# Kernel optimization log

Measured on AMD Instinct MI355X. Metric: run time of the kernel, lower is better.

Reference implementation:

```python
import jax, jax.numpy as jnp
import numpy as np
import math

D_MODEL = 1024
N_HEADS = 16
D_HEAD = D_MODEL // N_HEADS
D_FF = 4 * D_MODEL
EPS = 1e-5


def layer_norm(x, gamma, beta):
    mu = jnp.mean(x, axis=-1, keepdims=True)
    var = jnp.var(x, axis=-1, keepdims=True)
    return (x - mu) * jax.lax.rsqrt(var + EPS) * gamma + beta


def setup_inputs() -> dict:
    key = jax.random.key(0)
    ks = jax.random.split(key, 8)
    B, C, D = 32, 256, D_MODEL
    s = 0.02
    return {
        "X": jax.random.normal(ks[0], (B, C, D), dtype=jnp.float32),
        "W_qkv": jax.random.normal(ks[1], (D, 3 * D), dtype=jnp.float32) * s,
        "b_qkv": jnp.zeros((3 * D,), dtype=jnp.float32),
        "W_proj": jax.random.normal(ks[2], (D, D), dtype=jnp.float32) * s,
        "b_proj": jnp.zeros((D,), dtype=jnp.float32),
        "g1": jnp.ones((D,), dtype=jnp.float32),
        "beta1": jnp.zeros((D,), dtype=jnp.float32),
        "g2": jnp.ones((D,), dtype=jnp.float32),
        "beta2": jnp.zeros((D,), dtype=jnp.float32),
        "W_ff1": jax.random.normal(ks[3], (D, D_FF), dtype=jnp.float32) * s,
        "b_ff1": jnp.zeros((D_FF,), dtype=jnp.float32),
        "W_ff2": jax.random.normal(ks[4], (D_FF, D), dtype=jnp.float32) * s,
        "b_ff2": jnp.zeros((D,), dtype=jnp.float32),
    }


def reference(X, W_qkv, b_qkv, W_proj, b_proj, g1, beta1, g2, beta2,
              W_ff1, b_ff1, W_ff2, b_ff2):
    B, C, D = X.shape
    H, Dh = N_HEADS, D_HEAD
    scale = 1.0 / math.sqrt(Dh)

    Xn = layer_norm(X, g1, beta1)
    qkv = Xn @ W_qkv + b_qkv                       # [B, C, 3D]
    q, k, v = jnp.split(qkv, 3, axis=-1)
    # split heads -> [B, H, C, Dh]
    sh = lambda t: t.reshape(B, C, H, Dh).transpose(0, 2, 1, 3)
    q, k, v = sh(q), sh(k), sh(v)

    scores = jnp.einsum("bhcd,bhkd->bhck", q, k) * scale  # [B, H, C, C]
    attn = jax.nn.softmax(scores, axis=-1)
    ctx = jnp.einsum("bhck,bhkd->bhcd", attn, v)           # [B, H, C, Dh]
    ctx = ctx.transpose(0, 2, 1, 3).reshape(B, C, D)

    X1 = X + (ctx @ W_proj + b_proj)
    X2n = layer_norm(X1, g2, beta2)
    h = jax.nn.gelu(X2n @ W_ff1 + b_ff1, approximate=False)
    X_out = X1 + (h @ W_ff2 + b_ff2)
    A = attn.mean(axis=1)                                   # [B, C, C]
    return (X_out, A)
```

## Files before the change

kernel.cpp:

```cpp
#include <hip/hip_runtime.h>
#include <cstdint>
#include <cstddef>

typedef short bf16x8 __attribute__((ext_vector_type(8)));
typedef float f32x4 __attribute__((ext_vector_type(4)));
typedef unsigned short u16;
typedef u16 u16x8 __attribute__((ext_vector_type(8)));

#define GLD16(gptr, lptr)                                                            \
  __builtin_amdgcn_global_load_lds((const __attribute__((address_space(1))) void*)(gptr), \
                                   (__attribute__((address_space(3))) void*)(lptr), 16, 0, 0)

__device__ __forceinline__ u16 f2bf(float f) {
  union { float f; unsigned u; } v; v.f = f;
  unsigned r = v.u + 0x7FFF + ((v.u >> 16) & 1);
  return (u16)(r >> 16);
}
__device__ __forceinline__ float bf2f(u16 h) {
  union { unsigned u; float f; } v; v.u = ((unsigned)h) << 16;
  return v.f;
}

__device__ __forceinline__ bf16x8 lds_read_sw64(const u16* base, int row, int col) {
  int byt = row * 128 + col * 2;
  byt ^= (row & 7) << 4;
  return *(const bf16x8*)((const char*)base + byt);
}

__global__ __launch_bounds__(256) void transpose_cast(const float* __restrict__ in,
                                                      u16* __restrict__ out, int R, int C) {
  __shared__ float tile[32][33];
  const int tx = threadIdx.x, ty = threadIdx.y;
  const int c0 = blockIdx.x * 32, r0 = blockIdx.y * 32;
#pragma unroll
  for (int i = 0; i < 32; i += 8)
    tile[ty + i][tx] = in[(size_t)(r0 + ty + i) * C + c0 + tx];
  __syncthreads();
#pragma unroll
  for (int i = 0; i < 32; i += 8)
    out[(size_t)(c0 + ty + i) * R + r0 + tx] = f2bf(tile[tx][ty + i]);
}

__global__ __launch_bounds__(256) void layernorm_bf16(const float* __restrict__ X,
                                                      const float* __restrict__ g,
                                                      const float* __restrict__ be,
                                                      u16* __restrict__ out) {
  const int row = blockIdx.x, t = threadIdx.x;
  const int lane = t & 63, wave = t >> 6;
  const float* x = X + (size_t)row * 1024;
  __shared__ float part[4];
  float v[4]; float s = 0.f;
#pragma unroll
  for (int i = 0; i < 4; ++i) { v[i] = x[t + i * 256]; s += v[i]; }
#pragma unroll
  for (int o = 32; o >= 1; o >>= 1) s += __shfl_xor(s, o);
  if (lane == 0) part[wave] = s;
  __syncthreads();
  const float mu = (part[0] + part[1] + part[2] + part[3]) * (1.f / 1024.f);
  float d2 = 0.f;
#pragma unroll
  for (int i = 0; i < 4; ++i) { float d = v[i] - mu; d2 += d * d; }
#pragma unroll
  for (int o = 32; o >= 1; o >>= 1) d2 += __shfl_xor(d2, o);
  __syncthreads();
  if (lane == 0) part[wave] = d2;
  __syncthreads();
  const float var = (part[0] + part[1] + part[2] + part[3]) * (1.f / 1024.f);
  const float rstd = rsqrtf(var + 1e-5f);
#pragma unroll
  for (int i = 0; i < 4; ++i) {
    const int c = t + i * 256;
    out[(size_t)row * 1024 + c] = f2bf((v[i] - mu) * rstd * g[c] + be[c]);
  }
}

template <int EPI>
__global__ __launch_bounds__(256, 2) void gemm_sb(const u16* __restrict__ A,
                                                  const u16* __restrict__ Bt,
                                                  const float* __restrict__ bias,
                                                  const float* __restrict__ res,
                                                  float* __restrict__ outf,
                                                  u16* __restrict__ outb,
                                                  int M, int N, int K) {
  constexpr int ABYT = 128 * 128;
  __shared__ __attribute__((aligned(16))) char lds[2 * ABYT];

  const int t = threadIdx.x, lane = t & 63, wave = t >> 6;
  const int wm = wave >> 1, wn = wave & 1;
  const int l15 = lane & 15, l16 = lane >> 4;

  const int xcd = (int)blockIdx.x & 7, q = (int)blockIdx.x >> 3;
  const int j = q & 63, gq = q >> 6;
  const int g = gq * 8 + xcd;
  const int NGN = N >> 10;
  const int gm = g / NGN, gn = g % NGN;
  const int bm = (gm * 8 + (j >> 3)) * 128;
  const int bn = (gn * 8 + (j & 7)) * 128;

  const u16* aptr[4];
  const u16* bptr[4];
#pragma unroll
  for (int c = 0; c < 4; ++c) {
    int Lb = c * 4096 + t * 16;
    int x = (Lb ^ ((Lb >> 3) & 0x70)) >> 1;
    aptr[c] = A + (size_t)(bm + (x >> 6)) * K + (x & 63);
    bptr[c] = Bt + (size_t)(bn + (x >> 6)) * K + (x & 63);
  }

  auto stage = [&](int p) {
    const int ko = p * 64;
    char* ab = lds + t * 16;
    char* bb = lds + ABYT + t * 16;
#pragma unroll
    for (int c = 0; c < 4; ++c) GLD16(aptr[c] + ko, ab + c * 4096);
#pragma unroll
    for (int c = 0; c < 4; ++c) GLD16(bptr[c] + ko, bb + c * 4096);
  };

  const int co0 = l16 * 16, co1 = 64 + l16 * 16;
  f32x4 acc[4][4] = {};
  const int nkt = K >> 6;

#pragma unroll 1
  for (int kt = 0; kt < nkt; ++kt) {
    __syncthreads();
    stage(kt);
    __syncthreads();

    const char* ab = lds;
    const char* bb = lds + ABYT;
#pragma unroll
    for (int ks = 0; ks < 2; ++ks) {
      const int co = ks ? co1 : co0;
      bf16x8 a[4], b[4];
#pragma unroll
      for (int m = 0; m < 4; ++m) {
        const int r = wm * 64 + m * 16 + l15;
        a[m] = *(const bf16x8*)(ab + r * 128 + (co ^ ((r & 7) << 4)));
      }
#pragma unroll
      for (int n = 0; n < 4; ++n) {
        const int r = wn * 64 + n * 16 + l15;
        b[n] = *(const bf16x8*)(bb + r * 128 + (co ^ ((r & 7) << 4)));
      }
#pragma unroll
      for (int m = 0; m < 4; ++m)
#pragma unroll
        for (int n = 0; n < 4; ++n)
          acc[m][n] = __builtin_amdgcn_mfma_f32_16x16x32_bf16(a[m], b[n], acc[m][n], 0, 0, 0);
    }
  }

  const int r0 = l16 * 4;
#pragma unroll
  for (int m = 0; m < 4; ++m) {
#pragma unroll
    for (int n = 0; n < 4; ++n) {
      const int col = bn + wn * 64 + n * 16 + l15;
      const float bv = bias[col];
#pragma unroll
      for (int r = 0; r < 4; ++r) {
        const int row = bm + wm * 64 + m * 16 + r0 + r;
        const float v = acc[m][n][r] + bv;
        const size_t o = (size_t)row * N + col;
        if (EPI == 0) {
          outb[o] = f2bf(v);
        } else if (EPI == 1) {
          outf[o] = res[o] + v;
        } else {
          const float u = 0.7978845608f * (v + 0.044715f * v * v * v);
          const float e = __expf(2.f * u);
          const float th = 1.f - 2.f / (1.f + e);
          outb[o] = f2bf(0.5f * v * (1.f + th));
        }
      }
    }
  }
}

__global__ __launch_bounds__(256) void attn_scores(const u16* __restrict__ qkv,
                                                   u16* __restrict__ probs) {
  __shared__ u16 Ks[256 * 64];
  __shared__ u16 Qs[64 * 64];
  const int t = threadIdx.x, lane = t & 63, wave = t >> 6;
  const int qb = blockIdx.x * 64, h = blockIdx.y, b = blockIdx.z;
  const size_t row0 = (size_t)b * 256 * 3072;

#pragma unroll
  for (int is = 0; is < 8; ++is) {
    int L = (is * 2048 + t * 8) * 2;
    int x = (L ^ ((L >> 3) & 0x70)) >> 1;
    int kk = x >> 6, d = x & 63;
    const u16* gp = qkv + row0 + (size_t)kk * 3072 + 1024 + h * 64 + d;
    GLD16(gp, (char*)Ks + is * 4096 + wave * 1024);
  }
#pragma unroll
  for (int is = 0; is < 2; ++is) {
    int L = (is * 2048 + t * 8) * 2;
    int x = (L ^ ((L >> 3) & 0x70)) >> 1;
    int q = x >> 6, d = x & 63;
    const u16* gp = qkv + row0 + (size_t)(qb + q) * 3072 + h * 64 + d;
    GLD16(gp, (char*)Qs + is * 4096 + wave * 1024);
  }
  __syncthreads();

  f32x4 acc[16] = {};
  bf16x8 aq[2];
#pragma unroll
  for (int ks = 0; ks < 2; ++ks)
    aq[ks] = lds_read_sw64(Qs, wave * 16 + (lane & 15), ks * 32 + (lane >> 4) * 8);
#pragma unroll
  for (int nf = 0; nf < 16; ++nf) {
#pragma unroll
    for (int ks = 0; ks < 2; ++ks) {
      bf16x8 bk = lds_read_sw64(Ks, nf * 16 + (lane & 15), ks * 32 + (lane >> 4) * 8);
      acc[nf] = __builtin_amdgcn_mfma_f32_16x16x32_bf16(aq[ks], bk, acc[nf], 0, 0, 0);
    }
  }

  const int r0 = (lane >> 4) * 4, cc = lane & 15;
  const float sc = 0.125f;
#pragma unroll
  for (int r = 0; r < 4; ++r) {
    float mx = -1e30f;
#pragma unroll
    for (int nf = 0; nf < 16; ++nf) mx = fmaxf(mx, acc[nf][r]);
#pragma unroll
    for (int o = 8; o >= 1; o >>= 1) mx = fmaxf(mx, __shfl_xor(mx, o));
    float s = 0.f;
#pragma unroll
    for (int nf = 0; nf < 16; ++nf) {
      float e = __expf((acc[nf][r] - mx) * sc);
      acc[nf][r] = e; s += e;
    }
#pragma unroll
    for (int o = 8; o >= 1; o >>= 1) s += __shfl_xor(s, o);
    const float rinv = 1.f / s;
    const int qrow = qb + wave * 16 + r0 + r;
    u16* prow = probs + (size_t)((b * 16 + h) * 256 + qrow) * 256;
#pragma unroll
    for (int nf = 0; nf < 16; ++nf)
      prow[nf * 16 + cc] = f2bf(acc[nf][r] * rinv);
  }
}

__global__ __launch_bounds__(256) void amean(const u16* __restrict__ probs,
                                             float* __restrict__ A) {
  const int bq = blockIdx.x;
  const int b = bq >> 8, q = bq & 255;
  const int t = threadIdx.x;
  float s = 0.f;
#pragma unroll
  for (int h = 0; h < 16; ++h)
    s += bf2f(probs[(size_t)((b * 16 + h) * 256 + q) * 256 + t]);
  A[(size_t)bq * 256 + t] = s * (1.f / 16.f);
}

__global__ __launch_bounds__(256) void attn_pv(const u16* __restrict__ qkv,
                                               const u16* __restrict__ probs,
                                               u16* __restrict__ ctx) {
  __shared__ u16 Vs[64 * 256];
  const int t = threadIdx.x, lane = t & 63, wave = t >> 6;
  const int h = blockIdx.x, b = blockIdx.y;

#pragma unroll
  for (int p = 0; p < 8; ++p) {
    int idx = p * 2048 + t * 8;
    int kk = idx >> 6, d0 = idx & 63;
    u16x8 vv = *(const u16x8*)(qkv + (size_t)(b * 256 + kk) * 3072 + 2048 + h * 64 + d0);
#pragma unroll
    for (int j = 0; j < 8; ++j) {
      int d = d0 + j;
      int byt = (d * 512 + kk * 2) ^ ((d & 7) << 4);
      *(u16*)((char*)Vs + byt) = vv[j];
    }
  }
  __syncthreads();

  f32x4 acc[4][4] = {};
  const u16* Pb = probs + (size_t)((b * 16 + h) * 256) * 256;
  const int cc = lane & 15, kg = (lane >> 4) * 8;
#pragma unroll
  for (int kt = 0; kt < 8; ++kt) {
    bf16x8 a[4], v[4];
#pragma unroll
    for (int m = 0; m < 4; ++m)
      a[m] = *(const bf16x8*)(Pb + (size_t)(wave * 64 + m * 16 + cc) * 256 + kt * 32 + kg);
#pragma unroll
    for (int n = 0; n < 4; ++n) {
      int d = n * 16 + cc;
      int kk = kt * 32 + kg;
      int byt = (d * 512 + kk * 2) ^ ((d & 7) << 4);
      v[n] = *(const bf16x8*)((const char*)Vs + byt);
    }
#pragma unroll
    for (int m = 0; m < 4; ++m)
#pragma unroll
      for (int n = 0; n < 4; ++n)
        acc[m][n] = __builtin_amdgcn_mfma_f32_16x16x32_bf16(a[m], v[n], acc[m][n], 0, 0, 0);
  }

  const int r0 = (lane >> 4) * 4;
#pragma unroll
  for (int m = 0; m < 4; ++m) {
    const int q = wave * 64 + m * 16 + r0;
#pragma unroll
    for (int n = 0; n < 4; ++n) {
      const int col = h * 64 + n * 16 + cc;
#pragma unroll
      for (int r = 0; r < 4; ++r)
        ctx[(size_t)(b * 256 + q + r) * 1024 + col] = f2bf(acc[m][n][r]);
    }
  }
}

extern "C" void kernel_launch(void* const* d_in, const int* in_sizes, int n_in,
                              void* d_out, int out_size, void* d_ws, size_t ws_size,
                              hipStream_t stream) {
  const float* X      = (const float*)d_in[0];
  const float* W_qkv  = (const float*)d_in[1];
  const float* b_qkv  = (const float*)d_in[2];
  const float* W_proj = (const float*)d_in[3];
  const float* b_proj = (const float*)d_in[4];
  const float* g1     = (const float*)d_in[5];
  const float* beta1  = (const float*)d_in[6];
  const float* g2     = (const float*)d_in[7];
  const float* beta2  = (const float*)d_in[8];
  const float* W_ff1  = (const float*)d_in[9];
  const float* b_ff1  = (const float*)d_in[10];
  const float* W_ff2  = (const float*)d_in[11];
  const float* b_ff2  = (const float*)d_in[12];

  float* Xout = (float*)d_out;
  float* Aout = (float*)d_out + 8388608;

  char* ws = (char*)d_ws;
  const size_t MB = 1u << 20;
  u16* xn    = (u16*)(ws + 0);
  u16* wqkv  = (u16*)(ws + 16 * MB);
  u16* wproj = (u16*)(ws + 22 * MB);
  u16* wff1  = (u16*)(ws + 24 * MB);
  u16* wff2  = (u16*)(ws + 32 * MB);
  u16* qkv   = (u16*)(ws + 40 * MB);
  u16* probs = (u16*)(ws + 88 * MB);
  u16* hbuf  = probs;
  float* x1  = (float*)(ws + 152 * MB);
  u16* ctx   = xn;
  u16* x1n   = xn;

  const dim3 tb(32, 8);
  transpose_cast<<<dim3(96, 32),  tb, 0, stream>>>(W_qkv,  wqkv, 1024, 3072);
  transpose_cast<<<dim3(32, 32),  tb, 0, stream>>>(W_proj, wproj, 1024, 1024);
  transpose_cast<<<dim3(128, 32), tb, 0, stream>>>(W_ff1,  wff1, 1024, 4096);
  transpose_cast<<<dim3(32, 128), tb, 0, stream>>>(W_ff2,  wff2, 4096, 1024);

  layernorm_bf16<<<8192, 256, 0, stream>>>(X, g1, beta1, xn);

  gemm_sb<0><<<1536, 256, 0, stream>>>(xn, wqkv, b_qkv, nullptr, nullptr, qkv,
                                       8192, 3072, 1024);

  attn_scores<<<dim3(4, 16, 32), 256, 0, stream>>>(qkv, probs);
  amean<<<8192, 256, 0, stream>>>(probs, Aout);
  attn_pv<<<dim3(16, 32), 256, 0, stream>>>(qkv, probs, ctx);

  gemm_sb<1><<<512, 256, 0, stream>>>(ctx, wproj, b_proj, X, x1, nullptr,
                                      8192, 1024, 1024);

  layernorm_bf16<<<8192, 256, 0, stream>>>(x1, g2, beta2, x1n);

  gemm_sb<2><<<2048, 256, 0, stream>>>(x1n, wff1, b_ff1, nullptr, nullptr, hbuf,
                                       8192, 4096, 1024);

  gemm_sb<1><<<512, 256, 0, stream>>>(hbuf, wff2, b_ff2, x1, Xout, nullptr,
                                      8192, 1024, 4096);
}
```

Baseline: 350.4 us.

## Add 256x256 ping-pong GEMM kernel for QKV and FF1 projections

Adds a new 512-thread GEMM with 256x256 output tiles and double-buffered LDS filled by direct global-to-LDS loads. The global loads for the next K tile are split across barrier-separated phases so they overlap the MFMA work, with raised priority around MFMA bursts. The kernel also remaps block indices for L2 locality. It replaces the 128x128 kernel for the QKV and FF1 GEMMs to increase data reuse per tile and reduce LDS/global traffic per flop. The cost is higher register pressure and fewer blocks per CU, and its hand-tuned waitcnt values have to match the issued loads exactly.

```diff
diff --git a/kernel.cpp b/kernel.cpp
--- a/kernel.cpp
+++ b/kernel.cpp
@@ -19,6 +19,16 @@
 __device__ __forceinline__ float bf2f(u16 h) {
   union { unsigned u; float f; } v; v.u = ((unsigned)h) << 16;
   return v.f;
+}
+
+template <int N> __device__ __forceinline__ void vmwait() {
+  if constexpr (N == 0) asm volatile("s_waitcnt vmcnt(0)" ::: "memory");
+  else if constexpr (N == 2) asm volatile("s_waitcnt vmcnt(2)" ::: "memory");
+  else asm volatile("s_waitcnt vmcnt(8)" ::: "memory");
+}
+
+__device__ __forceinline__ f32x4 mfma16(bf16x8 a, bf16x8 b, f32x4 c) {
+  return __builtin_amdgcn_mfma_f32_16x16x32_bf16(a, b, c, 0, 0, 0);
 }
 
 __device__ __forceinline__ bf16x8 lds_read_sw64(const u16* base, int row, int col) {
@@ -71,6 +81,158 @@
   for (int i = 0; i < 4; ++i) {
     const int c = t + i * 256;
     out[(size_t)row * 1024 + c] = f2bf((v[i] - mu) * rstd * g[c] + be[c]);
+  }
+}
+
+template <int EPI>
+__global__ __launch_bounds__(512, 2) void gemm_4p(const u16* __restrict__ A,
+                                                  const u16* __restrict__ Bt,
+                                                  const float* __restrict__ bias,
+                                                  const float* __restrict__ res,
+                                                  float* __restrict__ outf,
+                                                  u16* __restrict__ outb,
+                                                  int M, int N, int K) {
+  constexpr int TSZ = 256 * 128;
+  __shared__ __attribute__((aligned(16))) char lds[4 * TSZ];
+
+  const int t = threadIdx.x, lane = t & 63, wave = t >> 6;
+  const int wm = wave >> 2, wn = wave & 3;
+  const int l15 = lane & 15, l16 = lane >> 4;
+
+  const int lb = ((int)blockIdx.x & 7) * ((int)gridDim.x >> 3) + ((int)blockIdx.x >> 3);
+  const int NBN = N >> 8;
+  const int bm = (lb / NBN) * 256, bn = (lb % NBN) * 256;
+
+  const u16* aptr[4];
+  const u16* bptr[4];
+#pragma unroll
+  for (int u = 0; u < 4; ++u) {
+    int Lb = u * 8192 + t * 16;
+    int x = (Lb ^ ((Lb >> 3) & 0x70)) >> 1;
+    aptr[u] = A + (size_t)(bm + (x >> 6)) * K + (x & 63);
+    bptr[u] = Bt + (size_t)(bn + (x >> 6)) * K + (x & 63);
+  }
+  auto stA = [&](int p, int u) { GLD16(aptr[u] + p * 64, lds + (p & 1) * TSZ + u * 8192 + t * 16); };
+  auto stB = [&](int p, int u) { GLD16(bptr[u] + p * 64, lds + 2 * TSZ + (p & 1) * TSZ + u * 8192 + t * 16); };
+
+  stA(0, 0); stA(0, 2); stB(0, 0); stB(0, 1); stB(0, 2); stB(0, 3); stA(0, 1); stA(0, 3);
+
+  f32x4 acc[8][4] = {};
+  const int nkt = K >> 6;
+
+#pragma unroll 1
+  for (int kt = 0; kt < nkt; ++kt) {
+    const char* ab = lds + (kt & 1) * TSZ;
+    const char* bb = lds + 2 * TSZ + (kt & 1) * TSZ;
+    const bool st = (kt + 1 < nkt);
+    bf16x8 aF[4][2], b0[2][2], b1[2][2];
+
+    vmwait<2>();
+    asm volatile("s_barrier" ::: "memory");
+    if (st) { stA(kt + 1, 0); stA(kt + 1, 2); stB(kt + 1, 0); stB(kt + 1, 1); }
+#pragma unroll
+    for (int fm = 0; fm < 4; ++fm) {
+      const int r = wm * 128 + fm * 16 + l15;
+      const int rb = r * 128, sw = (r & 7) << 4;
+      aF[fm][0] = *(const bf16x8*)(ab + rb + ((l16 * 16) ^ sw));
+      aF[fm][1] = *(const bf16x8*)(ab + rb + ((64 + l16 * 16) ^ sw));
+    }
+#pragma unroll
+    for (int fn = 0; fn < 2; ++fn) {
+      const int r = wn * 64 + fn * 16 + l15;
+      const int rb = r * 128, sw = (r & 7) << 4;
+      b0[fn][0] = *(const bf16x8*)(bb + rb + ((l16 * 16) ^ sw));
+      b0[fn][1] = *(const bf16x8*)(bb + rb + ((64 + l16 * 16) ^ sw));
+    }
+    asm volatile("s_waitcnt lgkmcnt(0)" ::: "memory");
+    __builtin_amdgcn_sched_barrier(0);
+    __builtin_amdgcn_s_setprio(1);
+#pragma unroll
+    for (int ks = 0; ks < 2; ++ks)
+#pragma unroll
+      for (int fm = 0; fm < 4; ++fm)
+#pragma unroll
+        for (int fn = 0; fn < 2; ++fn)
+          acc[fm][fn] = mfma16(aF[fm][ks], b0[fn][ks], acc[fm][fn]);
+    __builtin_amdgcn_s_setprio(0);
+
+    asm volatile("s_barrier" ::: "memory");
+    if (st) { stB(kt + 1, 2); stB(kt + 1, 3); stA(kt + 1, 1); stA(kt + 1, 3); }
+#pragma unroll
+    for (int fn = 0; fn < 2; ++fn) {
+      const int r = wn * 64 + (2 + fn) * 16 + l15;
+      const int rb = r * 128, sw = (r & 7) << 4;
+      b1[fn][0] = *(const bf16x8*)(bb + rb + ((l16 * 16) ^ sw));
+      b1[fn][1] = *(const bf16x8*)(bb + rb + ((64 + l16 * 16) ^ sw));
+    }
+    asm volatile("s_waitcnt lgkmcnt(0)" ::: "memory");
+    __builtin_amdgcn_sched_barrier(0);
+    __builtin_amdgcn_s_setprio(1);
+#pragma unroll
+    for (int ks = 0; ks < 2; ++ks)
+#pragma unroll
+      for (int fm = 0; fm < 4; ++fm)
+#pragma unroll
+        for (int fn = 0; fn < 2; ++fn)
+          acc[fm][2 + fn] = mfma16(aF[fm][ks], b1[fn][ks], acc[fm][2 + fn]);
+    __builtin_amdgcn_s_setprio(0);
+
+    if (st) vmwait<8>(); else vmwait<0>();
+    asm volatile("s_barrier" ::: "memory");
+#pragma unroll
+    for (int fm = 0; fm < 4; ++fm) {
+      const int r = wm * 128 + (4 + fm) * 16 + l15;
+      const int rb = r * 128, sw = (r & 7) << 4;
+      aF[fm][0] = *(const bf16x8*)(ab + rb + ((l16 * 16) ^ sw));
+      aF[fm][1] = *(const bf16x8*)(ab + rb + ((64 + l16 * 16) ^ sw));
+    }
+    asm volatile("s_waitcnt lgkmcnt(0)" ::: "memory");
+    __builtin_amdgcn_sched_barrier(0);
+    __builtin_amdgcn_s_setprio(1);
+#pragma unroll
+    for (int ks = 0; ks < 2; ++ks)
+#pragma unroll
+      for (int fm = 0; fm < 4; ++fm)
+#pragma unroll
+        for (int fn = 0; fn < 2; ++fn)
+          acc[4 + fm][2 + fn] = mfma16(aF[fm][ks], b1[fn][ks], acc[4 + fm][2 + fn]);
+    __builtin_amdgcn_s_setprio(0);
+
+    __builtin_amdgcn_s_setprio(1);
+#pragma unroll
+    for (int ks = 0; ks < 2; ++ks)
+#pragma unroll
+      for (int fm = 0; fm < 4; ++fm)
+#pragma unroll
+        for (int fn = 0; fn < 2; ++fn)
+          acc[4 + fm][fn] = mfma16(aF[fm][ks], b0[fn][ks], acc[4 + fm][fn]);
+    __builtin_amdgcn_s_setprio(0);
+  }
+
+  const int r0 = l16 * 4;
+#pragma unroll
+  for (int fm = 0; fm < 8; ++fm) {
+#pragma unroll
+    for (int fn = 0; fn < 4; ++fn) {
+      const int col = bn + wn * 64 + fn * 16 + l15;
+      const float bv = bias[col];
+#pragma unroll
+      for (int r = 0; r < 4; ++r) {
+        const int row = bm + wm * 128 + fm * 16 + r0 + r;
+        const float v = acc[fm][fn][r] + bv;
+        const size_t o = (size_t)row * N + col;
+        if (EPI == 0) {
+          outb[o] = f2bf(v);
+        } else if (EPI == 1) {
+          outf[o] = res[o] + v;
+        } else {
+          const float u = 0.7978845608f * (v + 0.044715f * v * v * v);
+          const float e = __expf(2.f * u);
+          const float th = 1.f - 2.f / (1.f + e);
+          outb[o] = f2bf(0.5f * v * (1.f + th));
+        }
+      }
+    }
   }
 }
 
@@ -147,7 +309,7 @@
       for (int m = 0; m < 4; ++m)
 #pragma unroll
         for (int n = 0; n < 4; ++n)
-          acc[m][n] = __builtin_amdgcn_mfma_f32_16x16x32_bf16(a[m], b[n], acc[m][n], 0, 0, 0);
+          acc[m][n] = mfma16(a[m], b[n], acc[m][n]);
     }
   }
 
@@ -214,7 +376,7 @@
 #pragma unroll
     for (int ks = 0; ks < 2; ++ks) {
       bf16x8 bk = lds_read_sw64(Ks, nf * 16 + (lane & 15), ks * 32 + (lane >> 4) * 8);
-      acc[nf] = __builtin_amdgcn_mfma_f32_16x16x32_bf16(aq[ks], bk, acc[nf], 0, 0, 0);
+      acc[nf] = mfma16(aq[ks], bk, acc[nf]);
     }
   }
 
@@ -297,7 +459,7 @@
     for (int m = 0; m < 4; ++m)
 #pragma unroll
       for (int n = 0; n < 4; ++n)
-        acc[m][n] = __builtin_amdgcn_mfma_f32_16x16x32_bf16(a[m], v[n], acc[m][n], 0, 0, 0);
+        acc[m][n] = mfma16(a[m], v[n], acc[m][n]);
   }
 
   const int r0 = (lane >> 4) * 4;
@@ -356,8 +518,8 @@
 
   layernorm_bf16<<<8192, 256, 0, stream>>>(X, g1, beta1, xn);
 
-  gemm_sb<0><<<1536, 256, 0, stream>>>(xn, wqkv, b_qkv, nullptr, nullptr, qkv,
-                                       8192, 3072, 1024);
+  gemm_4p<0><<<384, 512, 0, stream>>>(xn, wqkv, b_qkv, nullptr, nullptr, qkv,
+                                      8192, 3072, 1024);
 
   attn_scores<<<dim3(4, 16, 32), 256, 0, stream>>>(qkv, probs);
   amean<<<8192, 256, 0, stream>>>(probs, Aout);
@@ -368,8 +530,8 @@
 
   layernorm_bf16<<<8192, 256, 0, stream>>>(x1, g2, beta2, x1n);
 
-  gemm_sb<2><<<2048, 256, 0, stream>>>(x1n, wff1, b_ff1, nullptr, nullptr, hbuf,
-                                       8192, 4096, 1024);
+  gemm_4p<2><<<512, 512, 0, stream>>>(x1n, wff1, b_ff1, nullptr, nullptr, hbuf,
+                                      8192, 4096, 1024);
 
   gemm_sb<1><<<512, 256, 0, stream>>>(hbuf, wff2, b_ff2, x1, Xout, nullptr,
                                       8192, 1024, 4096);
```

Result: slower. 357.4 us (+2.0%).

## Fuse attention scores, softmax, head-mean and PV into one per-query-block kernel

Applied to the files above, without the earlier changes.

Replaces the separate score/softmax, head-averaging and PV kernels with one kernel. Each block handles 32 queries of one batch and loops over all 16 heads, keeping probabilities in shared memory and accumulating the head mean in registers. This removes the global probability buffer round trip and two launches. K/Q/V for the next head are prefetched while the current head computes. In exchange there are far fewer blocks, heavier LDS use and several block barriers per head, which may limit occupancy and parallelism.

```diff
diff --git a/kernel.cpp b/kernel.cpp
--- a/kernel.cpp
+++ b/kernel.cpp
@@ -19,6 +19,10 @@
 __device__ __forceinline__ float bf2f(u16 h) {
   union { unsigned u; float f; } v; v.u = ((unsigned)h) << 16;
   return v.f;
+}
+
+__device__ __forceinline__ f32x4 mfma16(bf16x8 a, bf16x8 b, f32x4 c) {
+  return __builtin_amdgcn_mfma_f32_16x16x32_bf16(a, b, c, 0, 0, 0);
 }
 
 __device__ __forceinline__ bf16x8 lds_read_sw64(const u16* base, int row, int col) {
@@ -147,7 +151,7 @@
       for (int m = 0; m < 4; ++m)
 #pragma unroll
         for (int n = 0; n < 4; ++n)
-          acc[m][n] = __builtin_amdgcn_mfma_f32_16x16x32_bf16(a[m], b[n], acc[m][n], 0, 0, 0);
+          acc[m][n] = mfma16(a[m], b[n], acc[m][n]);
     }
   }
 
@@ -178,138 +182,169 @@
   }
 }
 
-__global__ __launch_bounds__(256) void attn_scores(const u16* __restrict__ qkv,
-                                                   u16* __restrict__ probs) {
+__global__ __launch_bounds__(256) void attn_fused(const u16* __restrict__ qkv,
+                                                  u16* __restrict__ ctx,
+                                                  float* __restrict__ Aout) {
   __shared__ u16 Ks[256 * 64];
-  __shared__ u16 Qs[64 * 64];
+  __shared__ u16 Vs[64 * 256];
+  __shared__ u16 Qs[32 * 64];
+  __shared__ u16 Ps[32 * 256];
+  __shared__ float red[2][2][32];
+
   const int t = threadIdx.x, lane = t & 63, wave = t >> 6;
-  const int qb = blockIdx.x * 64, h = blockIdx.y, b = blockIdx.z;
-  const size_t row0 = (size_t)b * 256 * 3072;
-
+  const int rg = wave & 1, kh = wave >> 1;
+  const int l15 = lane & 15, l16 = lane >> 4;
+  const int q0 = blockIdx.x * 32, b = blockIdx.y;
+  const size_t base = (size_t)b * 256 * 3072;
+
+  int kk_s[8], kd_s[8];
 #pragma unroll
   for (int is = 0; is < 8; ++is) {
     int L = (is * 2048 + t * 8) * 2;
     int x = (L ^ ((L >> 3) & 0x70)) >> 1;
-    int kk = x >> 6, d = x & 63;
-    const u16* gp = qkv + row0 + (size_t)kk * 3072 + 1024 + h * 64 + d;
-    GLD16(gp, (char*)Ks + is * 4096 + wave * 1024);
-  }
-#pragma unroll
-  for (int is = 0; is < 2; ++is) {
-    int L = (is * 2048 + t * 8) * 2;
-    int x = (L ^ ((L >> 3) & 0x70)) >> 1;
-    int q = x >> 6, d = x & 63;
-    const u16* gp = qkv + row0 + (size_t)(qb + q) * 3072 + h * 64 + d;
-    GLD16(gp, (char*)Qs + is * 4096 + wave * 1024);
-  }
-  __syncthreads();
-
-  f32x4 acc[16] = {};
-  bf16x8 aq[2];
-#pragma unroll
-  for (int ks = 0; ks < 2; ++ks)
-    aq[ks] = lds_read_sw64(Qs, wave * 16 + (lane & 15), ks * 32 + (lane >> 4) * 8);
-#pragma unroll
-  for (int nf = 0; nf < 16; ++nf) {
-#pragma unroll
-    for (int ks = 0; ks < 2; ++ks) {
-      bf16x8 bk = lds_read_sw64(Ks, nf * 16 + (lane & 15), ks * 32 + (lane >> 4) * 8);
-      acc[nf] = __builtin_amdgcn_mfma_f32_16x16x32_bf16(aq[ks], bk, acc[nf], 0, 0, 0);
-    }
-  }
-
-  const int r0 = (lane >> 4) * 4, cc = lane & 15;
-  const float sc = 0.125f;
-#pragma unroll
-  for (int r = 0; r < 4; ++r) {
-    float mx = -1e30f;
-#pragma unroll
-    for (int nf = 0; nf < 16; ++nf) mx = fmaxf(mx, acc[nf][r]);
-#pragma unroll
-    for (int o = 8; o >= 1; o >>= 1) mx = fmaxf(mx, __shfl_xor(mx, o));
-    float s = 0.f;
-#pragma unroll
-    for (int nf = 0; nf < 16; ++nf) {
-      float e = __expf((acc[nf][r] - mx) * sc);
-      acc[nf][r] = e; s += e;
-    }
-#pragma unroll
-    for (int o = 8; o >= 1; o >>= 1) s += __shfl_xor(s, o);
-    const float rinv = 1.f / s;
-    const int qrow = qb + wave * 16 + r0 + r;
-    u16* prow = probs + (size_t)((b * 16 + h) * 256 + qrow) * 256;
-#pragma unroll
-    for (int nf = 0; nf < 16; ++nf)
-      prow[nf * 16 + cc] = f2bf(acc[nf][r] * rinv);
-  }
-}
-
-__global__ __launch_bounds__(256) void amean(const u16* __restrict__ probs,
-                                             float* __restrict__ A) {
-  const int bq = blockIdx.x;
-  const int b = bq >> 8, q = bq & 255;
-  const int t = threadIdx.x;
-  float s = 0.f;
-#pragma unroll
-  for (int h = 0; h < 16; ++h)
-    s += bf2f(probs[(size_t)((b * 16 + h) * 256 + q) * 256 + t]);
-  A[(size_t)bq * 256 + t] = s * (1.f / 16.f);
-}
-
-__global__ __launch_bounds__(256) void attn_pv(const u16* __restrict__ qkv,
-                                               const u16* __restrict__ probs,
-                                               u16* __restrict__ ctx) {
-  __shared__ u16 Vs[64 * 256];
-  const int t = threadIdx.x, lane = t & 63, wave = t >> 6;
-  const int h = blockIdx.x, b = blockIdx.y;
-
-#pragma unroll
-  for (int p = 0; p < 8; ++p) {
-    int idx = p * 2048 + t * 8;
-    int kk = idx >> 6, d0 = idx & 63;
-    u16x8 vv = *(const u16x8*)(qkv + (size_t)(b * 256 + kk) * 3072 + 2048 + h * 64 + d0);
-#pragma unroll
-    for (int j = 0; j < 8; ++j) {
-      int d = d0 + j;
-      int byt = (d * 512 + kk * 2) ^ ((d & 7) << 4);
-      *(u16*)((char*)Vs + byt) = vv[j];
-    }
-  }
-  __syncthreads();
-
-  f32x4 acc[4][4] = {};
-  const u16* Pb = probs + (size_t)((b * 16 + h) * 256) * 256;
-  const int cc = lane & 15, kg = (lane >> 4) * 8;
-#pragma unroll
-  for (int kt = 0; kt < 8; ++kt) {
-    bf16x8 a[4], v[4];
-#pragma unroll
-    for (int m = 0; m < 4; ++m)
-      a[m] = *(const bf16x8*)(Pb + (size_t)(wave * 64 + m * 16 + cc) * 256 + kt * 32 + kg);
-#pragma unroll
-    for (int n = 0; n < 4; ++n) {
-      int d = n * 16 + cc;
-      int kk = kt * 32 + kg;
-      int byt = (d * 512 + kk * 2) ^ ((d & 7) << 4);
-      v[n] = *(const bf16x8*)((const char*)Vs + byt);
-    }
-#pragma unroll
-    for (int m = 0; m < 4; ++m)
-#pragma unroll
-      for (int n = 0; n < 4; ++n)
-        acc[m][n] = __builtin_amdgcn_mfma_f32_16x16x32_bf16(a[m], v[n], acc[m][n], 0, 0, 0);
-  }
-
-  const int r0 = (lane >> 4) * 4;
-#pragma unroll
-  for (int m = 0; m < 4; ++m) {
-    const int q = wave * 64 + m * 16 + r0;
-#pragma unroll
-    for (int n = 0; n < 4; ++n) {
-      const int col = h * 64 + n * 16 + cc;
-#pragma unroll
-      for (int r = 0; r < 4; ++r)
-        ctx[(size_t)(b * 256 + q + r) * 1024 + col] = f2bf(acc[m][n][r]);
+    kk_s[is] = x >> 6; kd_s[is] = x & 63;
+  }
+  int qr_s, qd_s;
+  { int L = t * 16; int x = (L ^ ((L >> 3) & 0x70)) >> 1; qr_s = x >> 6; qd_s = x & 63; }
+  int vkk[8], vd0[8];
+#pragma unroll
+  for (int p = 0; p < 8; ++p) { int idx = p * 2048 + t * 8; vkk[p] = idx >> 6; vd0[p] = idx & 63; }
+
+  auto stageKQ = [&](int h) {
+#pragma unroll
+    for (int is = 0; is < 8; ++is)
+      GLD16(qkv + base + (size_t)kk_s[is] * 3072 + 1024 + h * 64 + kd_s[is],
+            (char*)Ks + is * 4096 + wave * 1024);
+    GLD16(qkv + base + (size_t)(q0 + qr_s) * 3072 + h * 64 + qd_s,
+          (char*)Qs + wave * 1024);
+  };
+
+  u16x8 vvr[8];
+  stageKQ(0);
+#pragma unroll
+  for (int p = 0; p < 8; ++p)
+    vvr[p] = *(const u16x8*)(qkv + base + (size_t)vkk[p] * 3072 + 2048 + vd0[p]);
+
+  f32x4 A_acc[8] = {};
+
+#pragma unroll 1
+  for (int h = 0; h < 16; ++h) {
+    asm volatile("s_waitcnt vmcnt(0)" ::: "memory");
+    __syncthreads();
+
+#pragma unroll
+    for (int p = 0; p < 8; ++p) {
+#pragma unroll
+      for (int jj = 0; jj < 8; ++jj) {
+        const int d = vd0[p] + jj;
+        const int byt = (d * 512 + vkk[p] * 2) ^ ((d & 7) << 4);
+        *(u16*)((char*)Vs + byt) = vvr[p][jj];
+      }
+    }
+    if (h + 1 < 16) {
+#pragma unroll
+      for (int p = 0; p < 8; ++p)
+        vvr[p] = *(const u16x8*)(qkv + base + (size_t)vkk[p] * 3072 + 2048 + (h + 1) * 64 + vd0[p]);
+    }
+
+    f32x4 acc2[8] = {};
+    bf16x8 aq[2];
+#pragma unroll
+    for (int ks = 0; ks < 2; ++ks)
+      aq[ks] = lds_read_sw64(Qs, rg * 16 + l15, ks * 32 + l16 * 8);
+#pragma unroll
+    for (int nf = 0; nf < 8; ++nf) {
+#pragma unroll
+      for (int ks = 0; ks < 2; ++ks) {
+        bf16x8 bk = lds_read_sw64(Ks, (kh * 8 + nf) * 16 + l15, ks * 32 + l16 * 8);
+        acc2[nf] = mfma16(aq[ks], bk, acc2[nf]);
+      }
+    }
+
+    float mx[4], sm[4];
+#pragma unroll
+    for (int r = 0; r < 4; ++r) {
+      float m = -1e30f;
+#pragma unroll
+      for (int nf = 0; nf < 8; ++nf) m = fmaxf(m, acc2[nf][r]);
+#pragma unroll
+      for (int o = 8; o >= 1; o >>= 1) m = fmaxf(m, __shfl_xor(m, o));
+      mx[r] = m;
+    }
+    if (l15 == 0) {
+#pragma unroll
+      for (int r = 0; r < 4; ++r) red[0][kh][rg * 16 + l16 * 4 + r] = mx[r];
+    }
+    __syncthreads();
+#pragma unroll
+    for (int r = 0; r < 4; ++r) {
+      const int qr = rg * 16 + l16 * 4 + r;
+      const float gm = fmaxf(red[0][0][qr], red[0][1][qr]);
+      float s = 0.f;
+#pragma unroll
+      for (int nf = 0; nf < 8; ++nf) {
+        const float e = __expf((acc2[nf][r] - gm) * 0.125f);
+        acc2[nf][r] = e; s += e;
+      }
+#pragma unroll
+      for (int o = 8; o >= 1; o >>= 1) s += __shfl_xor(s, o);
+      sm[r] = s;
+    }
+    if (l15 == 0) {
+#pragma unroll
+      for (int r = 0; r < 4; ++r) red[1][kh][rg * 16 + l16 * 4 + r] = sm[r];
+    }
+    __syncthreads();
+
+#pragma unroll
+    for (int r = 0; r < 4; ++r) {
+      const int qr = rg * 16 + l16 * 4 + r;
+      const float rinv = 1.f / (red[1][0][qr] + red[1][1][qr]);
+#pragma unroll
+      for (int nf = 0; nf < 8; ++nf) {
+        const float p = acc2[nf][r] * rinv;
+        A_acc[nf][r] += p;
+        const int kcol = kh * 128 + nf * 16 + l15;
+        const int byt = (qr * 512 + kcol * 2) ^ ((qr & 7) << 4);
+        *(u16*)((char*)Ps + byt) = f2bf(p);
+      }
+    }
+    __syncthreads();
+    if (h + 1 < 16) stageKQ(h + 1);
+
+    f32x4 cacc[2] = {};
+#pragma unroll
+    for (int kt = 0; kt < 8; ++kt) {
+      const int prow = rg * 16 + l15;
+      const int pbyt = (prow * 512 + kt * 64 + l16 * 16) ^ ((prow & 7) << 4);
+      const bf16x8 a = *(const bf16x8*)((const char*)Ps + pbyt);
+#pragma unroll
+      for (int n = 0; n < 2; ++n) {
+        const int d = kh * 32 + n * 16 + l15;
+        const int kk = kt * 32 + l16 * 8;
+        const int vbyt = (d * 512 + kk * 2) ^ ((d & 7) << 4);
+        const bf16x8 v = *(const bf16x8*)((const char*)Vs + vbyt);
+        cacc[n] = mfma16(a, v, cacc[n]);
+      }
+    }
+#pragma unroll
+    for (int n = 0; n < 2; ++n) {
+      const int dcol = h * 64 + kh * 32 + n * 16 + l15;
+#pragma unroll
+      for (int r = 0; r < 4; ++r) {
+        const int qr = rg * 16 + l16 * 4 + r;
+        ctx[(size_t)(b * 256 + q0 + qr) * 1024 + dcol] = f2bf(cacc[n][r]);
+      }
+    }
+  }
+
+#pragma unroll
+  for (int nf = 0; nf < 8; ++nf) {
+    const int kcol = kh * 128 + nf * 16 + l15;
+#pragma unroll
+    for (int r = 0; r < 4; ++r) {
+      const int qr = rg * 16 + l16 * 4 + r;
+      Aout[(size_t)(b * 256 + q0 + qr) * 256 + kcol] = A_acc[nf][r] * (1.f / 16.f);
     }
   }
 }
@@ -342,8 +377,7 @@
   u16* wff1  = (u16*)(ws + 24 * MB);
   u16* wff2  = (u16*)(ws + 32 * MB);
   u16* qkv   = (u16*)(ws + 40 * MB);
-  u16* probs = (u16*)(ws + 88 * MB);
-  u16* hbuf  = probs;
+  u16* hbuf  = (u16*)(ws + 88 * MB);
   float* x1  = (float*)(ws + 152 * MB);
   u16* ctx   = xn;
   u16* x1n   = xn;
@@ -359,9 +393,7 @@
   gemm_sb<0><<<1536, 256, 0, stream>>>(xn, wqkv, b_qkv, nullptr, nullptr, qkv,
                                        8192, 3072, 1024);
 
-  attn_scores<<<dim3(4, 16, 32), 256, 0, stream>>>(qkv, probs);
-  amean<<<8192, 256, 0, stream>>>(probs, Aout);
-  attn_pv<<<dim3(16, 32), 256, 0, stream>>>(qkv, probs, ctx);
+  attn_fused<<<dim3(8, 32), 256, 0, stream>>>(qkv, ctx, Aout);
 
   gemm_sb<1><<<512, 256, 0, stream>>>(ctx, wproj, b_proj, X, x1, nullptr,
                                       8192, 1024, 1024);
```

New measurement: 381.9 us. 9.0% more time.
